# Optimization experiments

Hardware: AMD Instinct MI355X
Metric: run time of the kernel (lower is better)

Reference implementation:

```python
import jax, jax.numpy as jnp
import numpy as np

EPS = 1e-5
K = 20
THRESH = 0.5

def _bn_relu(x, g, b, m, v):
    # eval-mode BatchNorm1d followed by ReLU
    return jax.nn.relu(g * (x - m) * jax.lax.rsqrt(v + EPS) + b)

def setup_inputs() -> dict:
    key = jax.random.key(0)
    ks = jax.random.split(key, 16)
    T, C, CI, E, NC = 16384, 256, 8, 5, 13
    B, N = 2, T // 2
    inp = {
        "f_sem": jax.random.normal(ks[0], (T, C), jnp.float32),
        "f_ins": jax.random.normal(ks[1], (T, CI), jnp.float32),
        # equal-size, sorted batch assignment (2 clouds of 8192 points)
        "batch": jnp.repeat(jnp.arange(B, dtype=jnp.int64), N),
        # semantic_adaptation_fc: Linear(C,C) + BN + ReLU
        "W_sem": jax.random.normal(ks[2], (C, C), jnp.float32) * (1.0 / np.sqrt(C)),
        "b_sem": jnp.zeros((C,), jnp.float32),
        "g_sem": jnp.ones((C,), jnp.float32),
        "beta_sem": jnp.zeros((C,), jnp.float32),
        "m_sem": jax.random.normal(ks[3], (C,), jnp.float32) * 0.1,
        "v_sem": jax.random.uniform(ks[4], (C,), jnp.float32, 0.5, 1.5),
        # inst_fc: Linear(8,C) + BN + ReLU
        "W_ins": jax.random.normal(ks[5], (CI, C), jnp.float32) * (1.0 / np.sqrt(CI)),
        "b_ins": jnp.zeros((C,), jnp.float32),
        "g_ins": jnp.ones((C,), jnp.float32),
        "beta_ins": jnp.zeros((C,), jnp.float32),
        "m_ins": jax.random.normal(ks[6], (C,), jnp.float32) * 0.1,
        "v_ins": jax.random.uniform(ks[7], (C,), jnp.float32, 0.5, 1.5),
        # instance_embedding_fc: plain Linear(C,E)
        "W_emb": jax.random.normal(ks[8], (C, E), jnp.float32) * (1.0 / np.sqrt(C)),
        "b_emb": jnp.zeros((E,), jnp.float32),
        # classifier_fc: plain Linear(C,NC)
        "W_cls": jax.random.normal(ks[9], (C, NC), jnp.float32) * (1.0 / np.sqrt(C)),
        "b_cls": jnp.zeros((NC,), jnp.float32),
    }
    return inp

def _instance_fusion(e_ins, f_sem, batch):
    # assumes sorted batch with equal-size segments (enforced by setup_inputs)
    T, C = f_sem.shape
    B = int(batch[-1]) + 1
    N = T // B
    e = e_ins.reshape(B, N, -1)
    f = f_sem.reshape(B, N, C)
    # squared Euclidean pairwise distances per cloud: [B, N, N]
    sq = jnp.sum(e * e, axis=-1)
    d2 = sq[:, :, None] + sq[:, None, :] - 2.0 * jnp.einsum("bnd,bmd->bnm", e, e)
    d2 = jnp.maximum(d2, 0.0)
    neg_vals, idx = jax.lax.top_k(-d2, K)          # k smallest distances, [B,N,K]
    within = (-neg_vals) <= THRESH * THRESH        # distance <= threshold
    self_idx = jnp.broadcast_to(jnp.arange(N)[None, :, None], idx.shape)
    col = jnp.where(within, idx, self_idx)         # fall back to self outside threshold
    neigh = jax.vmap(lambda fb, cb: fb[cb])(f, col)  # [B,N,K,C]
    return jnp.max(neigh, axis=2).reshape(T, C)      # scatter-max == max over neighbors

def reference(f_sem, f_ins, batch,
              W_sem, b_sem, g_sem, beta_sem, m_sem, v_sem,
              W_ins, b_ins, g_ins, beta_ins, m_ins, v_ins,
              W_emb, b_emb, W_cls, b_cls):
    f_sem_prime = _bn_relu(f_sem @ W_sem + b_sem, g_sem, beta_sem, m_sem, v_sem)
    f_ins_h = _bn_relu(f_ins @ W_ins + b_ins, g_ins, beta_ins, m_ins, v_ins)
    f_sins = f_ins_h + f_sem_prime
    e_ins = f_sins @ W_emb + b_emb
    f_isem = _instance_fusion(e_ins, f_sem, batch)
    p_sem = f_isem @ W_cls + b_cls
    return (p_sem, e_ins)
```

## Files before the change

kernel.cpp:

```cpp
#include <hip/hip_runtime.h>
#include <math.h>

#define T 16384
#define C 256
#define CI 8
#define EDIM 5
#define NC 13
#define NPTS 8192
#define KNN 20
#define CAP 256
#define FR 32
#define FRPB 8
#define NCVT 256

typedef float f4v __attribute__((ext_vector_type(4)));
typedef _Float16 h8 __attribute__((ext_vector_type(8)));
typedef _Float16 h4v __attribute__((ext_vector_type(4)));

__global__ __launch_bounds__(256) void front_kernel(
    const float* __restrict__ f_sem, const float* __restrict__ f_ins,
    const float* __restrict__ W_sem, const float* __restrict__ b_sem,
    const float* __restrict__ g_sem, const float* __restrict__ beta_sem,
    const float* __restrict__ m_sem, const float* __restrict__ v_sem,
    const float* __restrict__ W_ins, const float* __restrict__ b_ins,
    const float* __restrict__ g_ins, const float* __restrict__ beta_ins,
    const float* __restrict__ m_ins, const float* __restrict__ v_ins,
    const float* __restrict__ W_emb, const float* __restrict__ b_emb,
    float* __restrict__ eA, double* __restrict__ eD,
    float* __restrict__ out_e, _Float16* __restrict__ fsem_h)
{
    const int nFront = T / FR;
    if (blockIdx.x >= nFront) {
        const size_t total = (size_t)T * C;
        const size_t stride = (size_t)NCVT * 256 * 8;
        size_t i = ((size_t)(blockIdx.x - nFront) * 256 + threadIdx.x) * 8;
        for (; i < total; i += stride) {
            const float4 a = *(const float4*)(f_sem + i);
            const float4 b = *(const float4*)(f_sem + i + 4);
            h8 h;
            h[0] = (_Float16)a.x; h[1] = (_Float16)a.y;
            h[2] = (_Float16)a.z; h[3] = (_Float16)a.w;
            h[4] = (_Float16)b.x; h[5] = (_Float16)b.y;
            h[6] = (_Float16)b.z; h[7] = (_Float16)b.w;
            *(h8*)(fsem_h + i) = h;
        }
        return;
    }

    __shared__ __align__(16) _Float16 sAh[FR][264];
    __shared__ __align__(16) _Float16 sAl[FR][264];
    __shared__ float bnA1[C], bnB1[C], bnA2[C], bnB2[C];
    __shared__ float weL[C][EDIM];
    __shared__ float lfi[FR][CI];
    __shared__ float sP[4][FR][EDIM];

    const int tid = threadIdx.x;
    const int rowBase = blockIdx.x * FR;

    #pragma unroll
    for (int i = 0; i < 8; i++) {
        const int idx = tid + 256 * i;
        const int g = idx * 4;
        const int row = g >> 8, k = g & 255;
        const float4 v = *(const float4*)(f_sem + (size_t)rowBase * C + g);
        const float vv[4] = {v.x, v.y, v.z, v.w};
        #pragma unroll
        for (int q = 0; q < 4; q++) {
            const _Float16 h = (_Float16)vv[q];
            sAh[row][k + q] = h;
            sAl[row][k + q] = (_Float16)(vv[q] - (float)h);
        }
    }
    {
        const int c = tid;
        const float rs1 = 1.0f / sqrtf(v_sem[c] + 1e-5f);
        const float A1 = g_sem[c] * rs1;
        bnA1[c] = A1;
        bnB1[c] = A1 * (b_sem[c] - m_sem[c]) + beta_sem[c];
        const float rs2 = 1.0f / sqrtf(v_ins[c] + 1e-5f);
        const float A2 = g_ins[c] * rs2;
        bnA2[c] = A2;
        bnB2[c] = A2 * (b_ins[c] - m_ins[c]) + beta_ins[c];
        #pragma unroll
        for (int j = 0; j < EDIM; j++) weL[c][j] = W_emb[c * EDIM + j];
    }
    if (tid < FR * CI) lfi[tid >> 3][tid & 7] = f_ins[rowBase * CI + tid];
    __syncthreads();

    const int w = tid >> 6, lane = tid & 63;
    const int r16 = lane & 15, kq = lane >> 4;
    const int n0 = 64 * w;

    f4v acc[2][4];
    #pragma unroll
    for (int mi = 0; mi < 2; mi++)
        #pragma unroll
        for (int ni = 0; ni < 4; ni++) acc[mi][ni] = (f4v){0.f, 0.f, 0.f, 0.f};

    for (int kt = 0; kt < 8; kt++) {
        const int koff = 32 * kt + 8 * kq;
        const h8 ah0 = *(const h8*)&sAh[r16][koff];
        const h8 ah1 = *(const h8*)&sAh[r16 + 16][koff];
        const h8 al0 = *(const h8*)&sAl[r16][koff];
        const h8 al1 = *(const h8*)&sAl[r16 + 16][koff];
        #pragma unroll
        for (int ni = 0; ni < 4; ni++) {
            const float* wp = W_sem + (size_t)koff * C + (n0 + 16 * ni + r16);
            float wf[8];
            #pragma unroll
            for (int j = 0; j < 8; j++) wf[j] = wp[(size_t)j * C];
            h8 bh, bl;
            #pragma unroll
            for (int j = 0; j < 8; j++) {
                const _Float16 h = (_Float16)wf[j];
                bh[j] = h;
                bl[j] = (_Float16)(wf[j] - (float)h);
            }
            acc[0][ni] = __builtin_amdgcn_mfma_f32_16x16x32_f16(ah0, bh, acc[0][ni], 0, 0, 0);
            acc[1][ni] = __builtin_amdgcn_mfma_f32_16x16x32_f16(ah1, bh, acc[1][ni], 0, 0, 0);
            acc[0][ni] = __builtin_amdgcn_mfma_f32_16x16x32_f16(al0, bh, acc[0][ni], 0, 0, 0);
            acc[1][ni] = __builtin_amdgcn_mfma_f32_16x16x32_f16(al1, bh, acc[1][ni], 0, 0, 0);
            acc[0][ni] = __builtin_amdgcn_mfma_f32_16x16x32_f16(ah0, bl, acc[0][ni], 0, 0, 0);
            acc[1][ni] = __builtin_amdgcn_mfma_f32_16x16x32_f16(ah1, bl, acc[1][ni], 0, 0, 0);
        }
    }

    f4v prow, pcol;
    {
        const f4v z = {0.f, 0.f, 0.f, 0.f};
        h8 ra, rb, ca, cb;
        #pragma unroll
        for (int j = 0; j < 8; j++) {
            ra[j] = (_Float16)(float)r16;
            rb[j] = (_Float16)((kq == 0 && j == 0) ? 1.0f : 0.0f);
            ca[j] = rb[j];
            cb[j] = ra[j];
        }
        prow = __builtin_amdgcn_mfma_f32_16x16x32_f16(ra, rb, z, 0, 0, 0);
        pcol = __builtin_amdgcn_mfma_f32_16x16x32_f16(ca, cb, z, 0, 0, 0);
    }
    const int colm = (int)pcol[0];
    int rloc[4];
    #pragma unroll
    for (int r = 0; r < 4; r++) rloc[r] = (int)prow[r];

    float p[2][4][EDIM];
    #pragma unroll
    for (int mi = 0; mi < 2; mi++)
        #pragma unroll
        for (int r = 0; r < 4; r++)
            #pragma unroll
            for (int j = 0; j < EDIM; j++) p[mi][r][j] = 0.f;

    #pragma unroll
    for (int ni = 0; ni < 4; ni++) {
        const int c = n0 + 16 * ni + colm;
        const float A1 = bnA1[c], B1 = bnB1[c];
        const float A2 = bnA2[c], B2 = bnB2[c];
        float wi[CI], we[EDIM];
        #pragma unroll
        for (int k = 0; k < CI; k++) wi[k] = W_ins[k * C + c];
        #pragma unroll
        for (int j = 0; j < EDIM; j++) we[j] = weL[c][j];
        #pragma unroll
        for (int mi = 0; mi < 2; mi++)
            #pragma unroll
            for (int r = 0; r < 4; r++) {
                const int row = 16 * mi + rloc[r];
                float x2 = 0.f;
                #pragma unroll
                for (int k = 0; k < CI; k++) x2 = fmaf(lfi[row][k], wi[k], x2);
                const float h1 = fmaxf(fmaf(A1, acc[mi][ni][r], B1), 0.f);
                const float h2 = fmaxf(fmaf(A2, x2, B2), 0.f);
                const float s = h1 + h2;
                #pragma unroll
                for (int j = 0; j < EDIM; j++) p[mi][r][j] = fmaf(s, we[j], p[mi][r][j]);
            }
    }

    #pragma unroll
    for (int off = 1; off < 16; off <<= 1)
        #pragma unroll
        for (int mi = 0; mi < 2; mi++)
            #pragma unroll
            for (int r = 0; r < 4; r++)
                #pragma unroll
                for (int j = 0; j < EDIM; j++)
                    p[mi][r][j] += __shfl_xor(p[mi][r][j], off);

    if (r16 == 0) {
        #pragma unroll
        for (int mi = 0; mi < 2; mi++)
            #pragma unroll
            for (int r = 0; r < 4; r++)
                #pragma unroll
                for (int j = 0; j < EDIM; j++)
                    sP[w][16 * mi + rloc[r]][j] = p[mi][r][j];
    }
    __syncthreads();

    if (tid < FR) {
        const int row = rowBase + tid;
        double sq = 0.0;
        #pragma unroll
        for (int j = 0; j < EDIM; j++) {
            const float s = ((sP[0][tid][j] + sP[1][tid][j]) +
                             (sP[2][tid][j] + sP[3][tid][j])) + b_emb[j];
            const double ed = (double)s;
            eD[(size_t)row * 8 + j] = ed;
            sq = fma(ed, ed, sq);
            eA[(size_t)row * 8 + j] = s;
            out_e[(size_t)row * EDIM + j] = s;
        }
        eD[(size_t)row * 8 + 5] = sq;
        eA[(size_t)row * 8 + 5] = (float)sq;
        eA[(size_t)row * 8 + 6] = 0.f;
        eA[(size_t)row * 8 + 7] = 0.f;
    }
}

__device__ __attribute__((noinline)) float4 rescan_topk(
    const float* __restrict__ eA, const float* __restrict__ f_sem,
    const float* __restrict__ reRow, int cbase, int lane)
{
    float re0 = reRow[0], re1 = reRow[1], re2 = reRow[2];
    float re3 = reRow[3], re4 = reRow[4], sqF = reRow[5];
    float4 mx = make_float4(-3.4e38f, -3.4e38f, -3.4e38f, -3.4e38f);
    long long last = -1;
    for (int sel = 0; sel < KNN; sel++) {
        long long best = 0x7fffffffffffffffLL;
        for (int cb = 0; cb < NPTS; cb += 64) {
            const int j = cbase + cb + lane;
            const float4 ea = *(const float4*)(eA + (size_t)j * 8);
            const float2 eb = *(const float2*)(eA + (size_t)j * 8 + 4);
            float dot = re0 * ea.x;
            dot = fmaf(re1, ea.y, dot); dot = fmaf(re2, ea.z, dot);
            dot = fmaf(re3, ea.w, dot); dot = fmaf(re4, eb.x, dot);
            const float d2 = fmaxf((sqF + eb.y) - 2.f * dot, 0.f);
            long long key = (((long long)__float_as_uint(d2)) << 32)
                            | (unsigned int)(cb + lane);
            if (key <= last) key = 0x7fffffffffffffffLL;
            if (key < best) best = key;
        }
        #pragma unroll
        for (int off = 32; off; off >>= 1) {
            const long long o = __shfl_xor(best, off);
            if (o < best) best = o;
        }
        last = best;
        const int idx = (int)(best & 0xffffffffLL);
        const float4 fv = *(const float4*)(f_sem + (size_t)(cbase + idx) * C + lane * 4);
        mx.x = fmaxf(mx.x, fv.x); mx.y = fmaxf(mx.y, fv.y);
        mx.z = fmaxf(mx.z, fv.z); mx.w = fmaxf(mx.w, fv.w);
    }
    return mx;
}

template <bool H16>
__global__ __launch_bounds__(256) void knn_kernel(
    const float* __restrict__ eA, const double* __restrict__ eD,
    const float* __restrict__ f_sem, const _Float16* __restrict__ fsem_h,
    const float* __restrict__ W_cls, const float* __restrict__ b_cls,
    float* __restrict__ out_p)
{
    __shared__ float rA[FRPB][8];
    __shared__ double rD[FRPB][6];
    __shared__ unsigned short cidx[FRPB][CAP];
    __shared__ unsigned long long kP[FRPB][CAP];
    __shared__ int cntS[FRPB];
    __shared__ unsigned short memL[FRPB][24];
    __shared__ int nlS[FRPB];

    const int tid = threadIdx.x;
    const int rowBase = blockIdx.x * FRPB;

    if (tid < FRPB * 8) rA[tid >> 3][tid & 7] = eA[(rowBase + (tid >> 3)) * 8 + (tid & 7)];
    if (tid < FRPB * 6) rD[tid / 6][tid % 6] = eD[(rowBase + tid / 6) * 8 + tid % 6];
    if (tid < FRPB) cntS[tid] = 0;
    __syncthreads();

    const int wave = tid >> 6, lane = tid & 63;
    const int cbase = (rowBase >= NPTS) ? NPTS : 0;

    {
        float re[FRPB][5], thrb[FRPB];
        #pragma unroll
        for (int r = 0; r < FRPB; r++) {
            #pragma unroll
            for (int q = 0; q < 5; q++) re[r][q] = rA[r][q];
            thrb[r] = (rA[r][5] - 0.251f) * 0.5f;
        }

        const int cstart = wave * (NPTS / 4);
        for (int cb = cstart; cb < cstart + NPTS / 4; cb += 128) {
            const int j0 = cbase + cb + lane;
            const float4 ea0 = *(const float4*)(eA + (size_t)j0 * 8);
            const float2 eb0 = *(const float2*)(eA + (size_t)j0 * 8 + 4);
            const float4 ea1 = *(const float4*)(eA + (size_t)(j0 + 64) * 8);
            const float2 eb1 = *(const float2*)(eA + (size_t)(j0 + 64) * 8 + 4);
            const float hs0 = 0.5f * eb0.y, hs1 = 0.5f * eb1.y;
            #pragma unroll
            for (int r = 0; r < FRPB; r++) {
                float dot = re[r][0] * ea0.x;
                dot = fmaf(re[r][1], ea0.y, dot); dot = fmaf(re[r][2], ea0.z, dot);
                dot = fmaf(re[r][3], ea0.w, dot); dot = fmaf(re[r][4], eb0.x, dot);
                if (dot >= (thrb[r] + hs0)) {
                    const int pos = atomicAdd(&cntS[r], 1);
                    if (pos < CAP) cidx[r][pos] = (unsigned short)(cb + lane);
                }
            }
            #pragma unroll
            for (int r = 0; r < FRPB; r++) {
                float dot = re[r][0] * ea1.x;
                dot = fmaf(re[r][1], ea1.y, dot); dot = fmaf(re[r][2], ea1.z, dot);
                dot = fmaf(re[r][3], ea1.w, dot); dot = fmaf(re[r][4], eb1.x, dot);
                if (dot >= (thrb[r] + hs1)) {
                    const int pos = atomicAdd(&cntS[r], 1);
                    if (pos < CAP) cidx[r][pos] = (unsigned short)(cb + 64 + lane);
                }
            }
        }
    }
    __syncthreads();

    const int lr0 = 2 * wave, lr1 = lr0 + 1;

    #pragma unroll 1
    for (int rr = 0; rr < 2; rr++) {
        const int lr = lr0 + rr;
        const int cnt = cntS[lr];
        const double* rd = rD[lr];

        if (cnt <= CAP) {
            unsigned long long mykp[4];
            int myid[4], mpos[4];
            bool mem[4];
            #pragma unroll
            for (int q = 0; q < 4; q++) {
                const int i = lane + 64 * q;
                mykp[q] = ~0ull; myid[q] = -1; mem[q] = false;
                if (i < cnt) {
                    const int id = (int)cidx[lr][i];
                    const double* ep = eD + (size_t)(cbase + id) * 8;
                    double dotd = 0.0;
                    #pragma unroll
                    for (int qq = 0; qq < 5; qq++) dotd = fma(rd[qq], ep[qq], dotd);
                    const double d2 = fmax((rd[5] + ep[5]) - 2.0 * dotd, 0.0);
                    if (d2 <= 0.25) {
                        mem[q] = true;
                        const unsigned int k32 = __float_as_uint((float)d2);
                        mykp[q] = (((unsigned long long)k32) << 16) | (unsigned int)id;
                        myid[q] = id;
                    }
                }
            }
            int base = 0;
            #pragma unroll
            for (int q = 0; q < 4; q++) {
                const unsigned long long b = __ballot(mem[q]);
                if (mem[q]) {
                    const int pos = base + (int)__builtin_amdgcn_mbcnt_hi(
                        (unsigned int)(b >> 32),
                        __builtin_amdgcn_mbcnt_lo((unsigned int)b, 0u));
                    mpos[q] = pos;
                    kP[lr][pos] = mykp[q];
                }
                base += (int)__popcll(b);
            }
            const int m = base;

            if (m <= KNN) {
                #pragma unroll
                for (int q = 0; q < 4; q++)
                    if (mem[q]) memL[lr][mpos[q]] = (unsigned short)myid[q];
                if (lane == 0) nlS[lr] = m;
            } else {
                int rank[4] = {0, 0, 0, 0};
                for (int j = 0; j < m; j++) {
                    const unsigned long long kj = kP[lr][j];
                    #pragma unroll
                    for (int q = 0; q < 4; q++) rank[q] += (kj < mykp[q]) ? 1 : 0;
                }
                int sbase = 0;
                #pragma unroll
                for (int q = 0; q < 4; q++) {
                    const bool sel = mem[q] && (rank[q] < KNN);
                    const unsigned long long b = __ballot(sel);
                    if (sel) {
                        const int pos = sbase + (int)__builtin_amdgcn_mbcnt_hi(
                            (unsigned int)(b >> 32),
                            __builtin_amdgcn_mbcnt_lo((unsigned int)b, 0u));
                        memL[lr][pos] = (unsigned short)myid[q];
                    }
                    sbase += (int)__popcll(b);
                }
                if (lane == 0) nlS[lr] = sbase;
            }
        } else {
            if (lane == 0) { memL[lr][0] = 0; nlS[lr] = -1; }
        }
    }

    const int s0 = nlS[lr0], s1 = nlS[lr1];
    const bool fb0 = (s0 < 0), fb1 = (s1 < 0);
    const int n0 = fb0 ? 1 : s0, n1 = fb1 ? 1 : s1;
    float4 mx0 = make_float4(-3.4e38f, -3.4e38f, -3.4e38f, -3.4e38f);
    float4 mx1 = mx0;
    const int nmax = (n0 > n1) ? n0 : n1;

    if (H16) {
        for (int k = 0; k < nmax; k += 8) {
            int a[8], c[8];
            #pragma unroll
            for (int i = 0; i < 8; i++) {
                a[i] = (int)memL[lr0][(k + i < n0) ? k + i : n0 - 1];
                c[i] = (int)memL[lr1][(k + i < n1) ? k + i : n1 - 1];
            }
            h4v fa[8], fc[8];
            #pragma unroll
            for (int i = 0; i < 8; i++) {
                fa[i] = *(const h4v*)(fsem_h + (size_t)(cbase + a[i]) * C + lane * 4);
                fc[i] = *(const h4v*)(fsem_h + (size_t)(cbase + c[i]) * C + lane * 4);
            }
            #pragma unroll
            for (int i = 0; i < 8; i++) {
                mx0.x = fmaxf(mx0.x, (float)fa[i][0]);
                mx0.y = fmaxf(mx0.y, (float)fa[i][1]);
                mx0.z = fmaxf(mx0.z, (float)fa[i][2]);
                mx0.w = fmaxf(mx0.w, (float)fa[i][3]);
                mx1.x = fmaxf(mx1.x, (float)fc[i][0]);
                mx1.y = fmaxf(mx1.y, (float)fc[i][1]);
                mx1.z = fmaxf(mx1.z, (float)fc[i][2]);
                mx1.w = fmaxf(mx1.w, (float)fc[i][3]);
            }
        }
    } else {
        for (int k = 0; k < nmax; k += 4) {
            const int a0 = (int)memL[lr0][(k     < n0) ? k     : n0 - 1];
            const int a1 = (int)memL[lr0][(k + 1 < n0) ? k + 1 : n0 - 1];
            const int a2 = (int)memL[lr0][(k + 2 < n0) ? k + 2 : n0 - 1];
            const int a3 = (int)memL[lr0][(k + 3 < n0) ? k + 3 : n0 - 1];
            const int c0 = (int)memL[lr1][(k     < n1) ? k     : n1 - 1];
            const int c1 = (int)memL[lr1][(k + 1 < n1) ? k + 1 : n1 - 1];
            const int c2 = (int)memL[lr1][(k + 2 < n1) ? k + 2 : n1 - 1];
            const int c3 = (int)memL[lr1][(k + 3 < n1) ? k + 3 : n1 - 1];
            const float4 f0 = *(const float4*)(f_sem + (size_t)(cbase + a0) * C + lane * 4);
            const float4 f1 = *(const float4*)(f_sem + (size_t)(cbase + a1) * C + lane * 4);
            const float4 f2 = *(const float4*)(f_sem + (size_t)(cbase + a2) * C + lane * 4);
            const float4 f3 = *(const float4*)(f_sem + (size_t)(cbase + a3) * C + lane * 4);
            const float4 g0 = *(const float4*)(f_sem + (size_t)(cbase + c0) * C + lane * 4);
            const float4 g1 = *(const float4*)(f_sem + (size_t)(cbase + c1) * C + lane * 4);
            const float4 g2 = *(const float4*)(f_sem + (size_t)(cbase + c2) * C + lane * 4);
            const float4 g3 = *(const float4*)(f_sem + (size_t)(cbase + c3) * C + lane * 4);
            mx0.x = fmaxf(fmaxf(fmaxf(mx0.x, f0.x), fmaxf(f1.x, f2.x)), f3.x);
            mx0.y = fmaxf(fmaxf(fmaxf(mx0.y, f0.y), fmaxf(f1.y, f2.y)), f3.y);
            mx0.z = fmaxf(fmaxf(fmaxf(mx0.z, f0.z), fmaxf(f1.z, f2.z)), f3.z);
            mx0.w = fmaxf(fmaxf(fmaxf(mx0.w, f0.w), fmaxf(f1.w, f2.w)), f3.w);
            mx1.x = fmaxf(fmaxf(fmaxf(mx1.x, g0.x), fmaxf(g1.x, g2.x)), g3.x);
            mx1.y = fmaxf(fmaxf(fmaxf(mx1.y, g0.y), fmaxf(g1.y, g2.y)), g3.y);
            mx1.z = fmaxf(fmaxf(fmaxf(mx1.z, g0.z), fmaxf(g1.z, g2.z)), g3.z);
            mx1.w = fmaxf(fmaxf(fmaxf(mx1.w, g0.w), fmaxf(g1.w, g2.w)), g3.w);
        }
    }
    if (fb0) mx0 = rescan_topk(eA, f_sem, rA[lr0], cbase, lane);
    if (fb1) mx1 = rescan_topk(eA, f_sem, rA[lr1], cbase, lane);

    #pragma unroll 1
    for (int rr = 0; rr < 2; rr++) {
        const float4 mx = rr ? mx1 : mx0;
        float p[NC];
        #pragma unroll
        for (int k = 0; k < NC; k++) p[k] = 0.f;
        const float* w0 = W_cls + (4 * lane + 0) * NC;
        const float* w1 = W_cls + (4 * lane + 1) * NC;
        const float* w2 = W_cls + (4 * lane + 2) * NC;
        const float* w3 = W_cls + (4 * lane + 3) * NC;
        #pragma unroll
        for (int k = 0; k < NC; k++)
            p[k] = fmaf(mx.x, w0[k], fmaf(mx.y, w1[k], fmaf(mx.z, w2[k], fmaf(mx.w, w3[k], p[k]))));
        #pragma unroll
        for (int off = 32; off; off >>= 1)
            #pragma unroll
            for (int k = 0; k < NC; k++) p[k] += __shfl_xor(p[k], off);
        if (lane == 0) {
            const int row = rowBase + lr0 + rr;
            #pragma unroll
            for (int k = 0; k < NC; k++) out_p[row * NC + k] = p[k] + b_cls[k];
        }
    }
}

extern "C" void kernel_launch(void* const* d_in, const int* in_sizes, int n_in,
                              void* d_out, int out_size, void* d_ws, size_t ws_size,
                              hipStream_t stream) {
    (void)in_sizes; (void)n_in; (void)out_size;
    const float* f_sem    = (const float*)d_in[0];
    const float* f_ins    = (const float*)d_in[1];
    const float* W_sem    = (const float*)d_in[3];
    const float* b_sem    = (const float*)d_in[4];
    const float* g_sem    = (const float*)d_in[5];
    const float* beta_sem = (const float*)d_in[6];
    const float* m_sem    = (const float*)d_in[7];
    const float* v_sem    = (const float*)d_in[8];
    const float* W_ins    = (const float*)d_in[9];
    const float* b_ins    = (const float*)d_in[10];
    const float* g_ins    = (const float*)d_in[11];
    const float* beta_ins = (const float*)d_in[12];
    const float* m_ins    = (const float*)d_in[13];
    const float* v_ins    = (const float*)d_in[14];
    const float* W_emb    = (const float*)d_in[15];
    const float* b_emb    = (const float*)d_in[16];
    const float* W_cls    = (const float*)d_in[17];
    const float* b_cls    = (const float*)d_in[18];
    float* outp = (float*)d_out;

    char* ws = (char*)d_ws;
    float*    eA     = (float*)ws;
    double*   eD     = (double*)(ws + (size_t)T * 8 * 4);
    _Float16* fsem_h = (_Float16*)(ws + (size_t)T * 8 * 12);

    const size_t need_h16 = (size_t)T * 8 * 12 + (size_t)T * C * 2;
    const bool h16 = (ws_size >= need_h16);

    const int nFront = T / FR;
    front_kernel<<<h16 ? nFront + NCVT : nFront, 256, 0, stream>>>(
        f_sem, f_ins, W_sem, b_sem, g_sem, beta_sem, m_sem, v_sem,
        W_ins, b_ins, g_ins, beta_ins, m_ins, v_ins, W_emb, b_emb,
        eA, eD, outp + T * NC, h16 ? fsem_h : (_Float16*)nullptr);
    if (h16)
        knn_kernel<true><<<T / FRPB, 256, 0, stream>>>(
            eA, eD, f_sem, fsem_h, W_cls, b_cls, outp);
    else
        knn_kernel<false><<<T / FRPB, 256, 0, stream>>>(
            eA, eD, f_sem, (const _Float16*)nullptr, W_cls, b_cls, outp);
}
```

Measured before the change: 167.9 us.

## Fuse fp16 conversion of f_sem into front GEMM blocks and halve row tile

Removes the separate conversion blocks that re-read f_sem to produce the fp16 copy, and instead writes the fp16 high part from the tile each GEMM block already loads into shared memory. The row tile per block drops from 32 to 16, so the grid doubles and each wave keeps one 16-row MFMA fragment instead of two. This saves one full read of f_sem and adds parallelism, but each block reloads and converts the W_sem slice for half as many rows, which doubles the total W_sem traffic and conversion work.

```diff
diff --git a/kernel.cpp b/kernel.cpp
--- a/kernel.cpp
+++ b/kernel.cpp
@@ -9,9 +9,8 @@
 #define NPTS 8192
 #define KNN 20
 #define CAP 256
-#define FR 32
+#define FR 16
 #define FRPB 8
-#define NCVT 256
 
 typedef float f4v __attribute__((ext_vector_type(4)));
 typedef _Float16 h8 __attribute__((ext_vector_type(8)));
@@ -29,24 +28,6 @@
     float* __restrict__ eA, double* __restrict__ eD,
     float* __restrict__ out_e, _Float16* __restrict__ fsem_h)
 {
-    const int nFront = T / FR;
-    if (blockIdx.x >= nFront) {
-        const size_t total = (size_t)T * C;
-        const size_t stride = (size_t)NCVT * 256 * 8;
-        size_t i = ((size_t)(blockIdx.x - nFront) * 256 + threadIdx.x) * 8;
-        for (; i < total; i += stride) {
-            const float4 a = *(const float4*)(f_sem + i);
-            const float4 b = *(const float4*)(f_sem + i + 4);
-            h8 h;
-            h[0] = (_Float16)a.x; h[1] = (_Float16)a.y;
-            h[2] = (_Float16)a.z; h[3] = (_Float16)a.w;
-            h[4] = (_Float16)b.x; h[5] = (_Float16)b.y;
-            h[6] = (_Float16)b.z; h[7] = (_Float16)b.w;
-            *(h8*)(fsem_h + i) = h;
-        }
-        return;
-    }
-
     __shared__ __align__(16) _Float16 sAh[FR][264];
     __shared__ __align__(16) _Float16 sAl[FR][264];
     __shared__ float bnA1[C], bnB1[C], bnA2[C], bnB2[C];
@@ -58,18 +39,22 @@
     const int rowBase = blockIdx.x * FR;
 
     #pragma unroll
-    for (int i = 0; i < 8; i++) {
+    for (int i = 0; i < 4; i++) {
         const int idx = tid + 256 * i;
         const int g = idx * 4;
         const int row = g >> 8, k = g & 255;
         const float4 v = *(const float4*)(f_sem + (size_t)rowBase * C + g);
         const float vv[4] = {v.x, v.y, v.z, v.w};
+        h4v hv;
         #pragma unroll
         for (int q = 0; q < 4; q++) {
             const _Float16 h = (_Float16)vv[q];
             sAh[row][k + q] = h;
             sAl[row][k + q] = (_Float16)(vv[q] - (float)h);
-        }
+            hv[q] = h;
+        }
+        if (fsem_h)
+            *(h4v*)(fsem_h + (size_t)(rowBase + row) * C + k) = hv;
     }
     {
         const int c = tid;
@@ -91,18 +76,14 @@
     const int r16 = lane & 15, kq = lane >> 4;
     const int n0 = 64 * w;
 
-    f4v acc[2][4];
+    f4v acc[4];
     #pragma unroll
-    for (int mi = 0; mi < 2; mi++)
-        #pragma unroll
-        for (int ni = 0; ni < 4; ni++) acc[mi][ni] = (f4v){0.f, 0.f, 0.f, 0.f};
+    for (int ni = 0; ni < 4; ni++) acc[ni] = (f4v){0.f, 0.f, 0.f, 0.f};
 
     for (int kt = 0; kt < 8; kt++) {
         const int koff = 32 * kt + 8 * kq;
-        const h8 ah0 = *(const h8*)&sAh[r16][koff];
-        const h8 ah1 = *(const h8*)&sAh[r16 + 16][koff];
-        const h8 al0 = *(const h8*)&sAl[r16][koff];
-        const h8 al1 = *(const h8*)&sAl[r16 + 16][koff];
+        const h8 ah = *(const h8*)&sAh[r16][koff];
+        const h8 al = *(const h8*)&sAl[r16][koff];
         #pragma unroll
         for (int ni = 0; ni < 4; ni++) {
             const float* wp = W_sem + (size_t)koff * C + (n0 + 16 * ni + r16);
@@ -116,12 +97,9 @@
                 bh[j] = h;
                 bl[j] = (_Float16)(wf[j] - (float)h);
             }
-            acc[0][ni] = __builtin_amdgcn_mfma_f32_16x16x32_f16(ah0, bh, acc[0][ni], 0, 0, 0);
-            acc[1][ni] = __builtin_amdgcn_mfma_f32_16x16x32_f16(ah1, bh, acc[1][ni], 0, 0, 0);
-            acc[0][ni] = __builtin_amdgcn_mfma_f32_16x16x32_f16(al0, bh, acc[0][ni], 0, 0, 0);
-            acc[1][ni] = __builtin_amdgcn_mfma_f32_16x16x32_f16(al1, bh, acc[1][ni], 0, 0, 0);
-            acc[0][ni] = __builtin_amdgcn_mfma_f32_16x16x32_f16(ah0, bl, acc[0][ni], 0, 0, 0);
-            acc[1][ni] = __builtin_amdgcn_mfma_f32_16x16x32_f16(ah1, bl, acc[1][ni], 0, 0, 0);
+            acc[ni] = __builtin_amdgcn_mfma_f32_16x16x32_f16(ah, bh, acc[ni], 0, 0, 0);
+            acc[ni] = __builtin_amdgcn_mfma_f32_16x16x32_f16(al, bh, acc[ni], 0, 0, 0);
+            acc[ni] = __builtin_amdgcn_mfma_f32_16x16x32_f16(ah, bl, acc[ni], 0, 0, 0);
         }
     }
 
@@ -144,13 +122,11 @@
     #pragma unroll
     for (int r = 0; r < 4; r++) rloc[r] = (int)prow[r];
 
-    float p[2][4][EDIM];
+    float p[4][EDIM];
     #pragma unroll
-    for (int mi = 0; mi < 2; mi++)
-        #pragma unroll
-        for (int r = 0; r < 4; r++)
-            #pragma unroll
-            for (int j = 0; j < EDIM; j++) p[mi][r][j] = 0.f;
+    for (int r = 0; r < 4; r++)
+        #pragma unroll
+        for (int j = 0; j < EDIM; j++) p[r][j] = 0.f;
 
     #pragma unroll
     for (int ni = 0; ni < 4; ni++) {
@@ -163,39 +139,33 @@
         #pragma unroll
         for (int j = 0; j < EDIM; j++) we[j] = weL[c][j];
         #pragma unroll
-        for (int mi = 0; mi < 2; mi++)
-            #pragma unroll
-            for (int r = 0; r < 4; r++) {
-                const int row = 16 * mi + rloc[r];
-                float x2 = 0.f;
-                #pragma unroll
-                for (int k = 0; k < CI; k++) x2 = fmaf(lfi[row][k], wi[k], x2);
-                const float h1 = fmaxf(fmaf(A1, acc[mi][ni][r], B1), 0.f);
-                const float h2 = fmaxf(fmaf(A2, x2, B2), 0.f);
-                const float s = h1 + h2;
-                #pragma unroll
-                for (int j = 0; j < EDIM; j++) p[mi][r][j] = fmaf(s, we[j], p[mi][r][j]);
-            }
+        for (int r = 0; r < 4; r++) {
+            const int row = rloc[r];
+            float x2 = 0.f;
+            #pragma unroll
+            for (int k = 0; k < CI; k++) x2 = fmaf(lfi[row][k], wi[k], x2);
+            const float h1 = fmaxf(fmaf(A1, acc[ni][r], B1), 0.f);
+            const float h2 = fmaxf(fmaf(A2, x2, B2), 0.f);
+            const float s = h1 + h2;
+            #pragma unroll
+            for (int j = 0; j < EDIM; j++) p[r][j] = fmaf(s, we[j], p[r][j]);
+        }
     }
 
     #pragma unroll
     for (int off = 1; off < 16; off <<= 1)
         #pragma unroll
-        for (int mi = 0; mi < 2; mi++)
-            #pragma unroll
-            for (int r = 0; r < 4; r++)
-                #pragma unroll
-                for (int j = 0; j < EDIM; j++)
-                    p[mi][r][j] += __shfl_xor(p[mi][r][j], off);
+        for (int r = 0; r < 4; r++)
+            #pragma unroll
+            for (int j = 0; j < EDIM; j++)
+                p[r][j] += __shfl_xor(p[r][j], off);
 
     if (r16 == 0) {
         #pragma unroll
-        for (int mi = 0; mi < 2; mi++)
-            #pragma unroll
-            for (int r = 0; r < 4; r++)
-                #pragma unroll
-                for (int j = 0; j < EDIM; j++)
-                    sP[w][16 * mi + rloc[r]][j] = p[mi][r][j];
+        for (int r = 0; r < 4; r++)
+            #pragma unroll
+            for (int j = 0; j < EDIM; j++)
+                sP[w][rloc[r]][j] = p[r][j];
     }
     __syncthreads();
 
@@ -522,8 +492,7 @@
     const size_t need_h16 = (size_t)T * 8 * 12 + (size_t)T * C * 2;
     const bool h16 = (ws_size >= need_h16);
 
-    const int nFront = T / FR;
-    front_kernel<<<h16 ? nFront + NCVT : nFront, 256, 0, stream>>>(
+    front_kernel<<<T / FR, 256, 0, stream>>>(
         f_sem, f_ins, W_sem, b_sem, g_sem, beta_sem, m_sem, v_sem,
         W_ins, b_ins, g_ins, beta_ins, m_ins, v_ins, W_emb, b_emb,
         eA, eD, outp + T * NC, h16 ? fsem_h : (_Float16*)nullptr);
```

Measured after the change: 171.5 us. +2.1%, slower.
